# Kernel tuning notes

Measured on AMD Instinct MI355X. Metric: run time of the kernel, lower is better.

## Reference

```python
import jax, jax.numpy as jnp
import numpy as np

N = 100000        # num nodes
E = 3200000       # num edges (avg degree 32)
F_IN = 256        # num_features
H = 8             # hidden_channels
C = 16            # num_classes
NEG_SLOPE = 0.2   # GATv2Conv default negative_slope


def setup_inputs() -> dict:
    key = jax.random.key(0)
    ks = jax.random.split(key, 14)
    s = 0.1
    return {
        "x": jax.random.normal(ks[0], (N, F_IN), dtype=jnp.float32),
        "edge_index": jax.random.randint(ks[1], (2, E), 0, N),
        # layer 1 (GATv2Conv: lin_l for source, lin_r for target, att vector, out bias)
        "Wl1": jax.random.normal(ks[2], (F_IN, H), jnp.float32) * s,
        "bl1": jnp.zeros((H,), jnp.float32),
        "Wr1": jax.random.normal(ks[3], (F_IN, H), jnp.float32) * s,
        "br1": jnp.zeros((H,), jnp.float32),
        "att1": jax.random.normal(ks[4], (H,), jnp.float32) * s,
        "bias1": jnp.zeros((H,), jnp.float32),
        # layer 2
        "Wl2": jax.random.normal(ks[5], (H, C), jnp.float32) * s,
        "bl2": jnp.zeros((C,), jnp.float32),
        "Wr2": jax.random.normal(ks[6], (H, C), jnp.float32) * s,
        "br2": jnp.zeros((C,), jnp.float32),
        "att2": jax.random.normal(ks[7], (C,), jnp.float32) * s,
        "bias2": jnp.zeros((C,), jnp.float32),
    }


def _gatv2_conv(x, src, dst, Wl, bl, Wr, br, att, bias, n):
    # PyG GATv2Conv (heads=1): x_l = lin_l(x) (source), x_r = lin_r(x) (target)
    xl = x @ Wl + bl                                   # [N, D]
    xr = x @ Wr + br                                   # [N, D]
    e = jax.nn.leaky_relu(xl[src] + xr[dst], NEG_SLOPE)  # [E+N, D]
    s = e @ att                                        # [E+N] attention logits
    # softmax over incoming edges of each target node (segment softmax)
    m = jax.ops.segment_max(s, dst, num_segments=n)
    ex = jnp.exp(s - m[dst])
    denom = jax.ops.segment_sum(ex, dst, num_segments=n)
    alpha = ex / denom[dst]                            # [E+N]
    out = jax.ops.segment_sum(xl[src] * alpha[:, None], dst, num_segments=n)
    return out + bias


def reference(x, edge_index, Wl1, bl1, Wr1, br1, att1, bias1,
              Wl2, bl2, Wr2, br2, att2, bias2):
    # add_self_loops=True (GATv2Conv default)
    loop = jnp.arange(N, dtype=edge_index.dtype)
    src = jnp.concatenate([edge_index[0], loop])
    dst = jnp.concatenate([edge_index[1], loop])
    h = jax.nn.relu(_gatv2_conv(x, src, dst, Wl1, bl1, Wr1, br1, att1, bias1, N))
    return _gatv2_conv(h, src, dst, Wl2, bl2, Wr2, br2, att2, bias2, N)
```

## Files before the change

### kernel.cpp

```cpp
#include <hip/hip_runtime.h>
#include <hip/hip_fp16.h>

#define NN 100000
#define NE 3200000
#define FIN 256
#define H1 8
#define C2 16
#define NEG 0.2f

#define BKT 64
#define NB 1563
#define NBP 1568
#define CAP 2560
#define SB 32
#define SBN 3136
#define FPS 49
#define SCAP 110000
#define P1B 1024
#define EPB1 3125
#define LINB 1563
#define P2CAP 3520

__global__ __launch_bounds__(512) void k_clr(int* __restrict__ g) {
    int i = blockIdx.x * 512 + threadIdx.x;
    if (i < SB + NBP) g[i] = 0;
}

__global__ __launch_bounds__(512) void k_b(
        const float* __restrict__ x,
        const float* __restrict__ Wl, const float* __restrict__ bl,
        const float* __restrict__ Wr, const float* __restrict__ br,
        float* __restrict__ xl1, float* __restrict__ xr1,
        const int* __restrict__ ei,
        int* __restrict__ gcur1, int* __restrict__ sup1) {
    __shared__ int smem[10240];
    int tid = threadIdx.x;
    int m = blockIdx.x % 5, d = blockIdx.x / 5;

    if (m >= 3) {
        int p1 = d * 2 + (m - 3);
        if (p1 >= P1B) return;
        int* buf  = smem;
        int* cnt  = smem + EPB1;
        int* nb   = cnt + SB;
        int* gb   = nb + SB;
        int base = p1 * EPB1;
        if (tid < SB) cnt[tid] = 0;
        int es[7], ed[7], rk[7];
        #pragma unroll
        for (int r = 0; r < 7; ++r) {
            int i = tid + r * 512;
            if (i < EPB1) { es[r] = ei[base + i]; ed[r] = ei[NE + base + i]; }
        }
        __syncthreads();
        #pragma unroll
        for (int r = 0; r < 7; ++r) {
            int i = tid + r * 512;
            if (i < EPB1) rk[r] = atomicAdd(&cnt[ed[r] / SBN], 1);
        }
        __syncthreads();
        if (tid < SB) {
            int v = cnt[tid], inc = v;
            #pragma unroll
            for (int off = 1; off < SB; off <<= 1) {
                int u = __shfl_up(inc, off, 64);
                if (tid >= off) inc += u;
            }
            nb[tid] = inc - v;
            gb[tid] = atomicAdd(&gcur1[tid], v);
        }
        __syncthreads();
        #pragma unroll
        for (int r = 0; r < 7; ++r) {
            int i = tid + r * 512;
            if (i < EPB1) {
                int s = ed[r] / SBN;
                buf[nb[s] + rk[r]] = ((ed[r] - s * SBN) << 17) | es[r];
            }
        }
        __syncthreads();
        for (int j = tid; j < EPB1; j += 512) {
            int s = 0;
            #pragma unroll
            for (int st = 16; st >= 1; st >>= 1) {
                int c = s + st;
                if (c < SB && nb[c] <= j) s = c;
            }
            int dst = gb[s] + (j - nb[s]);
            if (dst < SCAP) sup1[(size_t)s * SCAP + dst] = buf[j];
        }
    } else {
        int lb = d * 3 + m;
        if (lb >= LINB) return;
        int blkNode = lb * 64;
        float* xf   = (float*)smem;
        float* part = (float*)smem;
        int lane = tid & 63;
        int wq = __builtin_amdgcn_readfirstlane(tid >> 6);

        float accl[8] = {0,0,0,0,0,0,0,0}, accr[8] = {0,0,0,0,0,0,0,0};

        #pragma unroll
        for (int ph = 0; ph < 2; ++ph) {
            __syncthreads();
            #pragma unroll
            for (int pass = 0; pass < 4; ++pass) {
                int i = tid + pass * 512;
                int row = i >> 5, c4 = i & 31;
                int node = blkNode + row; if (node >= NN) node = NN - 1;
                float4 v = *(const float4*)(x + (size_t)node * FIN + ph * 128 + c4 * 4);
                *(float4*)&xf[row * 128 + ((c4 ^ (row & 7)) << 2)] = v;
            }
            __syncthreads();
            int kbase = ph * 128 + wq * 16;
            const float* wlp = Wl + kbase * 8;
            const float* wrp = Wr + kbase * 8;
            const float* xbase = &xf[lane * 128];
            int lsw = lane & 7;
            #pragma unroll
            for (int jq = 0; jq < 4; ++jq) {
                int f = wq * 4 + jq;
                float4 xv = *(const float4*)(xbase + ((f ^ lsw) << 2));
                float xa[4] = {xv.x, xv.y, xv.z, xv.w};
                #pragma unroll
                for (int r = 0; r < 4; ++r) {
                    int k = jq * 4 + r;
                    #pragma unroll
                    for (int h = 0; h < 8; ++h) {
                        accl[h] = fmaf(xa[r], wlp[k * 8 + h], accl[h]);
                        accr[h] = fmaf(xa[r], wrp[k * 8 + h], accr[h]);
                    }
                }
            }
        }
        __syncthreads();
        float* pw = part + (size_t)(wq * 64 + lane) * 20;
        *(float4*)(pw)      = make_float4(accl[0], accl[1], accl[2], accl[3]);
        *(float4*)(pw + 4)  = make_float4(accl[4], accl[5], accl[6], accl[7]);
        *(float4*)(pw + 8)  = make_float4(accr[0], accr[1], accr[2], accr[3]);
        *(float4*)(pw + 12) = make_float4(accr[4], accr[5], accr[6], accr[7]);
        __syncthreads();
        int n2 = tid >> 3, p = tid & 7;
        float s0 = 0.f, s1 = 0.f;
        #pragma unroll
        for (int w2 = 0; w2 < 8; ++w2) {
            const float* pr = part + (size_t)(w2 * 64 + n2) * 20 + p * 2;
            s0 += pr[0]; s1 += pr[1];
        }
        int node = blkNode + n2;
        if (node < NN) {
            int o = p * 2;
            if (o < 8) {
                s0 += bl[o]; s1 += bl[o + 1];
                *(float2*)(xl1 + (size_t)node * H1 + o) = make_float2(s0, s1);
            } else {
                s0 += br[o - 8]; s1 += br[o - 7];
                *(float2*)(xr1 + (size_t)node * H1 + (o - 8)) = make_float2(s0, s1);
            }
        }
    }
}

__global__ __launch_bounds__(512) void k_p2(const int* __restrict__ sup1,
                                            const int* __restrict__ gcur1,
                                            int* __restrict__ gcur2,
                                            int* __restrict__ bedges) {
    __shared__ int buf[P2CAP];
    __shared__ int cnt[FPS], nb[FPS], gb[FPS];
    int s   = blockIdx.x >> 5;
    int sub = blockIdx.x & 31;
    int tid = threadIdx.x;
    int total = gcur1[s]; if (total > SCAP) total = SCAP;
    int beg = (int)((long)total * sub / 32);
    int end = (int)((long)total * (sub + 1) / 32);
    int n = end - beg;
    const int* sp = sup1 + (size_t)s * SCAP + beg;
    if (tid < FPS) cnt[tid] = 0;
    int pk[7], rk[7];
    #pragma unroll
    for (int r = 0; r < 7; ++r) {
        int i = tid + r * 512;
        if (i < n) pk[r] = sp[i];
    }
    __syncthreads();
    #pragma unroll
    for (int r = 0; r < 7; ++r) {
        int i = tid + r * 512;
        if (i < n) rk[r] = atomicAdd(&cnt[(pk[r] >> 17) >> 6], 1);
    }
    __syncthreads();
    if (tid < 64) {
        int v = (tid < FPS) ? cnt[tid] : 0, inc = v;
        #pragma unroll
        for (int off = 1; off < 64; off <<= 1) {
            int u = __shfl_up(inc, off, 64);
            if (tid >= off) inc += u;
        }
        if (tid < FPS) {
            nb[tid] = inc - v;
            gb[tid] = atomicAdd(&gcur2[s * FPS + tid], v);
        }
    }
    __syncthreads();
    #pragma unroll
    for (int r = 0; r < 7; ++r) {
        int i = tid + r * 512;
        if (i < n) {
            int fb = (pk[r] >> 17) >> 6;
            buf[nb[fb] + rk[r]] = (((pk[r] >> 17) & 63) << 17) | (pk[r] & 0x1FFFF);
        }
    }
    __syncthreads();
    for (int j = tid; j < n; j += 512) {
        int fb = 0;
        #pragma unroll
        for (int st = 32; st >= 1; st >>= 1) {
            int c = fb + st;
            if (c < FPS && nb[c] <= j) fb = c;
        }
        int dst = gb[fb] + (j - nb[fb]);
        if (dst < CAP) bedges[(size_t)(s * FPS + fb) * CAP + dst] = buf[j];
    }
}

__global__ __launch_bounds__(512) void k_sortgat1(
        int* __restrict__ bedges, const int* __restrict__ gcur2,
        int* __restrict__ meta,
        const float* __restrict__ xl, const float* __restrict__ xr,
        const float* __restrict__ att, const float* __restrict__ bias,
        const float* __restrict__ Wl2, const float* __restrict__ bl2,
        const float* __restrict__ Wr2, const float* __restrict__ br2,
        __half* __restrict__ xl2, float* __restrict__ xr2) {
    __shared__ int sorted[CAP];
    __shared__ int hist[BKT], nbase[BKT];
    int bkt = blockIdx.x;
    int tid = threadIdx.x;
    int ecnt = gcur2[bkt]; if (ecnt > CAP) ecnt = CAP;
    int* be = bedges + (size_t)bkt * CAP;
    if (tid < BKT) hist[tid] = 0;
    __syncthreads();
    int pkc[5], rkc[5];
    {
        int r = 0;
        for (int i = tid; i < ecnt; i += 512, ++r) {
            pkc[r] = be[i];
            rkc[r] = atomicAdd(&hist[pkc[r] >> 17], 1);
        }
    }
    __syncthreads();
    if (tid < BKT) {
        int v = hist[tid], inc = v;
        #pragma unroll
        for (int off = 1; off < 64; off <<= 1) {
            int u = __shfl_up(inc, off, 64);
            if (tid >= off) inc += u;
        }
        nbase[tid] = inc - v;
        meta[bkt * BKT + tid] = ((inc - v) << 16) | v;
    }
    __syncthreads();
    {
        int r = 0;
        for (int i = tid; i < ecnt; i += 512, ++r) {
            int pk = pkc[r];
            int dl = pk >> 17;
            sorted[nbase[dl] + rkc[r]] = pk & 0x1FFFF;
        }
    }
    __syncthreads();
    for (int i = tid; i < ecnt; i += 512)
        be[i] = sorted[i];

    int lane = tid & 63, wave = tid >> 6;
    int grp  = lane >> 4;
    int l16  = lane & 15;
    int q    = l16 & 1;
    int eo   = l16 >> 1;

    float attq[4], biasq[4];
    #pragma unroll
    for (int j = 0; j < 4; ++j) { attq[j] = att[q * 4 + j]; biasq[j] = bias[q * 4 + j]; }
    float wl2c[H1], wr2c[H1];
    #pragma unroll
    for (int d = 0; d < H1; ++d) {
        wl2c[d] = Wl2[d * C2 + l16];
        wr2c[d] = Wr2[d * C2 + l16];
    }
    float bl2c = bl2[l16], br2c = br2[l16];

    #pragma unroll
    for (int np = 0; np < 2; ++np) {
        int n = np * 32 + wave * 4 + grp;
        int g = bkt * BKT + n;
        int gc = g < NN ? g : NN - 1;
        int deg = hist[n] + 1;
        int nb_ = nbase[n];

        float4 xr4 = ((const float4*)(xr + (size_t)gc * H1))[q];
        float xrq[4] = {xr4.x, xr4.y, xr4.z, xr4.w};

        float denom = 0.f;
        float acc[4] = {0.f, 0.f, 0.f, 0.f};
        int mc = (deg + 7) >> 3;

        for (int c = 0; c < mc; ++c) {
            int e = c * 8 + eo;
            int src = (e > 0 && e < deg) ? sorted[nb_ + e - 1] : gc;
            float4 v = ((const float4*)(xl + (size_t)src * H1))[q];
            float xa[4] = {v.x, v.y, v.z, v.w};
            float s = 0.f;
            #pragma unroll
            for (int j = 0; j < 4; ++j) {
                float w = xa[j] + xrq[j];
                w = fmaxf(w, NEG * w);
                s = fmaf(attq[j], w, s);
            }
            s += __shfl_xor(s, 1, 64);
            float ex = (e < deg) ? __expf(s) : 0.f;
            denom += ex;
            #pragma unroll
            for (int j = 0; j < 4; ++j)
                acc[j] = fmaf(ex, xa[j], acc[j]);
        }

        #pragma unroll
        for (int off = 2; off <= 8; off <<= 1) {
            denom += __shfl_xor(denom, off, 64);
            #pragma unroll
            for (int j = 0; j < 4; ++j)
                acc[j] += __shfl_xor(acc[j], off, 64);
        }
        float inv = 1.f / denom;

        float h[4];
        #pragma unroll
        for (int j = 0; j < 4; ++j)
            h[j] = fmaxf(acc[j] * inv + biasq[j], 0.f);
        float hd[H1];
        #pragma unroll
        for (int d = 0; d < H1; ++d)
            hd[d] = __shfl(h[d & 3], (lane & 0x30) + (d >> 2), 64);
        float al = bl2c, ar = br2c;
        #pragma unroll
        for (int d = 0; d < H1; ++d) {
            al = fmaf(hd[d], wl2c[d], al);
            ar = fmaf(hd[d], wr2c[d], ar);
        }
        if (g < NN) {
            xl2[(size_t)g * C2 + l16] = __float2half(al);
            xr2[(size_t)g * C2 + l16] = ar;
        }
    }
}

__global__ __launch_bounds__(128) void k_gat2L(
        const int* __restrict__ sorted_g, const int* __restrict__ meta,
        const __half* __restrict__ xl, const float* __restrict__ xr,
        const float* __restrict__ att, const float* __restrict__ bias,
        float* __restrict__ out) {
    int wv = (blockIdx.x * 128 + threadIdx.x) >> 6;
    int lane = threadIdx.x & 63;
    int grp = lane >> 4;
    int l16 = lane & 15;
    int q = l16 & 3, eo = l16 >> 2;

    float attq[4], biasq[4];
    #pragma unroll
    for (int j = 0; j < 4; ++j) { attq[j] = att[q * 4 + j]; biasq[j] = bias[q * 4 + j]; }

    int g = wv * 4 + grp;
    int mt = meta[g];
    int deg = (mt & 0xFFFF) + 1;
    const int* sg = sorted_g + (size_t)(g >> 6) * CAP + (mt >> 16);

    float4 xr4 = ((const float4*)(xr + (size_t)g * C2))[q];
    float xrq[4] = {xr4.x, xr4.y, xr4.z, xr4.w};

    int dmax = deg;
    dmax = max(dmax, __shfl_xor(dmax, 16, 64));
    dmax = max(dmax, __shfl_xor(dmax, 32, 64));

    float denom = 0.f;
    float acc[4] = {0.f, 0.f, 0.f, 0.f};

    for (int e0 = 0; e0 < dmax; e0 += 4) {
        int e = e0 + eo;
        bool a = e < deg;
        int src = (e > 0 && a) ? sg[e - 1] : g;
        uint2 u = *(const uint2*)(xl + (size_t)src * C2 + q * 4);
        float2 fa = __half22float2(*(const __half2*)&u.x);
        float2 fb = __half22float2(*(const __half2*)&u.y);
        float xv[4] = {fa.x, fa.y, fb.x, fb.y};
        float s = 0.f;
        #pragma unroll
        for (int j = 0; j < 4; ++j) {
            float w = xv[j] + xrq[j];
            w = fmaxf(w, NEG * w);
            s = fmaf(attq[j], w, s);
        }
        s += __shfl_xor(s, 1, 64);
        s += __shfl_xor(s, 2, 64);
        float ex = a ? __expf(s) : 0.f;
        denom += ex;
        #pragma unroll
        for (int j = 0; j < 4; ++j)
            acc[j] = fmaf(ex, xv[j], acc[j]);
    }

    #pragma unroll
    for (int off = 4; off <= 8; off <<= 1) {
        denom += __shfl_xor(denom, off, 64);
        #pragma unroll
        for (int j = 0; j < 4; ++j)
            acc[j] += __shfl_xor(acc[j], off, 64);
    }
    float inv = 1.f / denom;

    if (eo == 0) {
        float4 r;
        r.x = acc[0] * inv + biasq[0];
        r.y = acc[1] * inv + biasq[1];
        r.z = acc[2] * inv + biasq[2];
        r.w = acc[3] * inv + biasq[3];
        ((float4*)(out + (size_t)g * C2))[q] = r;
    }
}

extern "C" void kernel_launch(void* const* d_in, const int* in_sizes, int n_in,
                              void* d_out, int out_size, void* d_ws, size_t ws_size,
                              hipStream_t stream) {
    const float* x     = (const float*)d_in[0];
    const int*   ei    = (const int*)d_in[1];
    const float* Wl1   = (const float*)d_in[2];
    const float* bl1   = (const float*)d_in[3];
    const float* Wr1   = (const float*)d_in[4];
    const float* br1   = (const float*)d_in[5];
    const float* att1  = (const float*)d_in[6];
    const float* bias1 = (const float*)d_in[7];
    const float* Wl2   = (const float*)d_in[8];
    const float* bl2   = (const float*)d_in[9];
    const float* Wr2   = (const float*)d_in[10];
    const float* br2   = (const float*)d_in[11];
    const float* att2  = (const float*)d_in[12];
    const float* bias2 = (const float*)d_in[13];
    float* out = (float*)d_out;

    int* bedges = (int*)d_ws;
    int* gcur1  = bedges + (size_t)NBP * CAP;
    int* gcur2  = gcur1 + SB;
    int* meta   = gcur2 + NBP;
    float* xl1  = (float*)(meta + NBP * BKT);
    float* xr1  = xl1 + (size_t)NN * H1;
    int* sup1   = (int*)(xr1 + (size_t)NN * H1);
    __half* xl2 = (__half*)sup1;
    float* xr2  = (float*)(xl2 + (size_t)NN * C2);

    k_clr<<<4, 512, 0, stream>>>(gcur1);
    k_b<<<2605, 512, 0, stream>>>(x, Wl1, bl1, Wr1, br1, xl1, xr1,
                                  ei, gcur1, sup1);
    k_p2<<<1024, 512, 0, stream>>>(sup1, gcur1, gcur2, bedges);
    k_sortgat1<<<NB, 512, 0, stream>>>(bedges, gcur2, meta, xl1, xr1, att1, bias1,
                                       Wl2, bl2, Wr2, br2, xl2, xr2);
    k_gat2L<<<12500, 128, 0, stream>>>(bedges, meta, xl2, xr2, att2, bias2, out);
}
```

Baseline: 113.3 us.

## Store layer-1 source features as fp16 and vectorize edge partition loads

```diff
diff --git a/kernel.cpp b/kernel.cpp
--- a/kernel.cpp
+++ b/kernel.cpp
@@ -16,8 +16,8 @@
 #define SBN 3136
 #define FPS 49
 #define SCAP 110000
-#define P1B 1024
-#define EPB1 3125
+#define P1B 800
+#define EPB1 4000
 #define LINB 1563
 #define P2CAP 3520
 
@@ -30,15 +30,15 @@
         const float* __restrict__ x,
         const float* __restrict__ Wl, const float* __restrict__ bl,
         const float* __restrict__ Wr, const float* __restrict__ br,
-        float* __restrict__ xl1, float* __restrict__ xr1,
+        __half* __restrict__ xl1, float* __restrict__ xr1,
         const int* __restrict__ ei,
         int* __restrict__ gcur1, int* __restrict__ sup1) {
     __shared__ int smem[10240];
     int tid = threadIdx.x;
-    int m = blockIdx.x % 5, d = blockIdx.x / 5;
-
-    if (m >= 3) {
-        int p1 = d * 2 + (m - 3);
+    int m = blockIdx.x % 3, d = blockIdx.x / 3;
+
+    if (m == 2) {
+        int p1 = d;
         if (p1 >= P1B) return;
         int* buf  = smem;
         int* cnt  = smem + EPB1;
@@ -46,17 +46,24 @@
         int* gb   = nb + SB;
         int base = p1 * EPB1;
         if (tid < SB) cnt[tid] = 0;
-        int es[7], ed[7], rk[7];
-        #pragma unroll
-        for (int r = 0; r < 7; ++r) {
-            int i = tid + r * 512;
-            if (i < EPB1) { es[r] = ei[base + i]; ed[r] = ei[NE + base + i]; }
-        }
-        __syncthreads();
-        #pragma unroll
-        for (int r = 0; r < 7; ++r) {
-            int i = tid + r * 512;
-            if (i < EPB1) rk[r] = atomicAdd(&cnt[ed[r] / SBN], 1);
+        int es[8], ed[8], rk[8];
+        int e0 = tid * 8;
+        bool act = e0 < EPB1;
+        if (act) {
+            int4 a = *(const int4*)(ei + base + e0);
+            int4 b = *(const int4*)(ei + base + e0 + 4);
+            es[0]=a.x; es[1]=a.y; es[2]=a.z; es[3]=a.w;
+            es[4]=b.x; es[5]=b.y; es[6]=b.z; es[7]=b.w;
+            int4 c = *(const int4*)(ei + NE + base + e0);
+            int4 e = *(const int4*)(ei + NE + base + e0 + 4);
+            ed[0]=c.x; ed[1]=c.y; ed[2]=c.z; ed[3]=c.w;
+            ed[4]=e.x; ed[5]=e.y; ed[6]=e.z; ed[7]=e.w;
+        }
+        __syncthreads();
+        if (act) {
+            #pragma unroll
+            for (int r = 0; r < 8; ++r)
+                rk[r] = atomicAdd(&cnt[ed[r] / SBN], 1);
         }
         __syncthreads();
         if (tid < SB) {
@@ -70,10 +77,9 @@
             gb[tid] = atomicAdd(&gcur1[tid], v);
         }
         __syncthreads();
-        #pragma unroll
-        for (int r = 0; r < 7; ++r) {
-            int i = tid + r * 512;
-            if (i < EPB1) {
+        if (act) {
+            #pragma unroll
+            for (int r = 0; r < 8; ++r) {
                 int s = ed[r] / SBN;
                 buf[nb[s] + rk[r]] = ((ed[r] - s * SBN) << 17) | es[r];
             }
@@ -90,7 +96,7 @@
             if (dst < SCAP) sup1[(size_t)s * SCAP + dst] = buf[j];
         }
     } else {
-        int lb = d * 3 + m;
+        int lb = d * 2 + m;
         if (lb >= LINB) return;
         int blkNode = lb * 64;
         float* xf   = (float*)smem;
@@ -152,7 +158,8 @@
             int o = p * 2;
             if (o < 8) {
                 s0 += bl[o]; s1 += bl[o + 1];
-                *(float2*)(xl1 + (size_t)node * H1 + o) = make_float2(s0, s1);
+                *(__half2*)(xl1 + (size_t)node * H1 + o) =
+                    __floats2half2_rn(s0, s1);
             } else {
                 s0 += br[o - 8]; s1 += br[o - 7];
                 *(float2*)(xr1 + (size_t)node * H1 + (o - 8)) = make_float2(s0, s1);
@@ -226,7 +233,7 @@
 __global__ __launch_bounds__(512) void k_sortgat1(
         int* __restrict__ bedges, const int* __restrict__ gcur2,
         int* __restrict__ meta,
-        const float* __restrict__ xl, const float* __restrict__ xr,
+        const __half* __restrict__ xl, const float* __restrict__ xr,
         const float* __restrict__ att, const float* __restrict__ bias,
         const float* __restrict__ Wl2, const float* __restrict__ bl2,
         const float* __restrict__ Wr2, const float* __restrict__ br2,
@@ -239,14 +246,22 @@
     int* be = bedges + (size_t)bkt * CAP;
     if (tid < BKT) hist[tid] = 0;
     __syncthreads();
-    int pkc[5], rkc[5];
-    {
-        int r = 0;
-        for (int i = tid; i < ecnt; i += 512, ++r) {
-            pkc[r] = be[i];
-            rkc[r] = atomicAdd(&hist[pkc[r] >> 17], 1);
-        }
-    }
+    int pkA[4], rkA[4], pkB = 0, rkB = 0;
+    int eA = tid * 4;
+    int nA = ecnt - eA; if (nA < 0) nA = 0; if (nA > 4) nA = 4;
+    if (nA == 4) {
+        int4 v = *(const int4*)(be + eA);
+        pkA[0]=v.x; pkA[1]=v.y; pkA[2]=v.z; pkA[3]=v.w;
+    } else {
+        for (int j = 0; j < nA; ++j) pkA[j] = be[eA + j];
+    }
+    int eB = 2048 + tid;
+    bool hasB = eB < ecnt;
+    if (hasB) pkB = be[eB];
+    #pragma unroll
+    for (int j = 0; j < 4; ++j)
+        if (j < nA) rkA[j] = atomicAdd(&hist[pkA[j] >> 17], 1);
+    if (hasB) rkB = atomicAdd(&hist[pkB >> 17], 1);
     __syncthreads();
     if (tid < BKT) {
         int v = hist[tid], inc = v;
@@ -259,17 +274,21 @@
         meta[bkt * BKT + tid] = ((inc - v) << 16) | v;
     }
     __syncthreads();
-    {
-        int r = 0;
-        for (int i = tid; i < ecnt; i += 512, ++r) {
-            int pk = pkc[r];
-            int dl = pk >> 17;
-            sorted[nbase[dl] + rkc[r]] = pk & 0x1FFFF;
-        }
-    }
-    __syncthreads();
-    for (int i = tid; i < ecnt; i += 512)
-        be[i] = sorted[i];
+    #pragma unroll
+    for (int j = 0; j < 4; ++j)
+        if (j < nA) {
+            int pk = pkA[j];
+            sorted[nbase[pk >> 17] + rkA[j]] = pk & 0x1FFFF;
+        }
+    if (hasB) sorted[nbase[pkB >> 17] + rkB] = pkB & 0x1FFFF;
+    __syncthreads();
+    if (nA == 4) {
+        int4 v = make_int4(sorted[eA], sorted[eA+1], sorted[eA+2], sorted[eA+3]);
+        *(int4*)(be + eA) = v;
+    } else {
+        for (int j = 0; j < nA; ++j) be[eA + j] = sorted[eA + j];
+    }
+    if (hasB) be[eB] = sorted[eB];
 
     int lane = tid & 63, wave = tid >> 6;
     int grp  = lane >> 4;
@@ -306,8 +325,10 @@
         for (int c = 0; c < mc; ++c) {
             int e = c * 8 + eo;
             int src = (e > 0 && e < deg) ? sorted[nb_ + e - 1] : gc;
-            float4 v = ((const float4*)(xl + (size_t)src * H1))[q];
-            float xa[4] = {v.x, v.y, v.z, v.w};
+            uint2 u = *(const uint2*)(xl + (size_t)src * H1 + q * 4);
+            float2 fa = __half22float2(*(const __half2*)&u.x);
+            float2 fb = __half22float2(*(const __half2*)&u.y);
+            float xa[4] = {fa.x, fa.y, fb.x, fb.y};
             float s = 0.f;
             #pragma unroll
             for (int j = 0; j < 4; ++j) {
@@ -449,14 +470,14 @@
     int* gcur1  = bedges + (size_t)NBP * CAP;
     int* gcur2  = gcur1 + SB;
     int* meta   = gcur2 + NBP;
-    float* xl1  = (float*)(meta + NBP * BKT);
-    float* xr1  = xl1 + (size_t)NN * H1;
+    __half* xl1 = (__half*)(meta + NBP * BKT);
+    float* xr1  = (float*)(xl1 + (size_t)NN * H1);
     int* sup1   = (int*)(xr1 + (size_t)NN * H1);
     __half* xl2 = (__half*)sup1;
     float* xr2  = (float*)(xl2 + (size_t)NN * C2);
 
     k_clr<<<4, 512, 0, stream>>>(gcur1);
-    k_b<<<2605, 512, 0, stream>>>(x, Wl1, bl1, Wr1, br1, xl1, xr1,
+    k_b<<<2400, 512, 0, stream>>>(x, Wl1, bl1, Wr1, br1, xl1, xr1,
                                   ei, gcur1, sup1);
     k_p2<<<1024, 512, 0, stream>>>(sup1, gcur1, gcur2, bedges);
     k_sortgat1<<<NB, 512, 0, stream>>>(bedges, gcur2, meta, xl1, xr1, att1, bias1,
```

Result: faster. 108.5 us, median of 2 (-4.3%).
